# Kernel tuning notes

Measured on AMD Instinct MI355X. Metric: run time of the kernel, lower is better.

The kernel has to match this reference:

```python
import jax, jax.numpy as jnp
import numpy as np

B, N, H, HEADS = 4, 4096, 256, 8
DEG = 16
E = B * N * DEG  # 262144 edges
DH = H // HEADS


def setup_inputs() -> dict:
    key = jax.random.key(0)
    ks = jax.random.split(key, 8)
    node_states = jax.random.normal(ks[0], (B, N, H), dtype=jnp.float32)
    # edge_indices rows: [batch_idx, target_node, source_node]
    b_idx = jnp.repeat(jnp.arange(B, dtype=jnp.int64), N * DEG)
    tgt = jnp.tile(jnp.repeat(jnp.arange(N, dtype=jnp.int64), DEG), B)
    src = jax.random.randint(ks[1], (E,), 0, N, dtype=jnp.int64)
    edge_indices = jnp.stack([b_idx, tgt, src])  # (3, E)
    s = 1.0 / np.sqrt(H)
    Wq = jax.random.normal(ks[2], (H, H), dtype=jnp.float32) * s
    Wk = jax.random.normal(ks[3], (H, H), dtype=jnp.float32) * s
    Wv = jax.random.normal(ks[4], (H, H), dtype=jnp.float32) * s
    bq = jnp.zeros((H,), dtype=jnp.float32)
    bk = jnp.zeros((H,), dtype=jnp.float32)
    bv = jnp.zeros((H,), dtype=jnp.float32)
    return {"node_states": node_states, "edge_indices": edge_indices,
            "Wq": Wq, "bq": bq, "Wk": Wk, "bk": bk, "Wv": Wv, "bv": bv}


def reference(node_states, edge_indices, Wq, bq, Wk, bk, Wv, bv):
    batch, n_nodes, hidden = node_states.shape
    b_idx, tgt, src = edge_indices[0], edge_indices[1], edge_indices[2]
    num_edges = b_idx.shape[0]

    # Dense Q/K/V projections on nodes (cheap), then per-edge gathers.
    Q = (node_states @ Wq + bq).reshape(batch, n_nodes, HEADS, DH)
    K = (node_states @ Wk + bk).reshape(batch, n_nodes, HEADS, DH)
    V = (node_states @ Wv + bv).reshape(batch, n_nodes, HEADS, DH)

    q_e = Q[b_idx, tgt]  # (E, heads, dh)
    k_e = K[b_idx, src]  # (E, heads, dh)
    scores = jnp.sum(q_e * k_e, axis=-1) / jnp.sqrt(jnp.float32(DH))  # (E, heads)

    # Segment softmax over source nodes, grouped per (batch, target) --
    # mirrors torch.sparse.softmax(logits, dim=-2).
    seg = b_idx * n_nodes + tgt  # (E,)
    num_seg = batch * n_nodes
    m = jax.ops.segment_max(scores, seg, num_segments=num_seg)  # (B*N, heads)
    exp = jnp.exp(scores - m[seg])
    denom = jax.ops.segment_sum(exp, seg, num_segments=num_seg)
    attn = exp / denom[seg]  # (E, heads)

    # Weighted scatter-sum of source values into target nodes
    # (replaces sparse edge_mask @ elwise_prod).
    v_e = V[b_idx, src]  # (E, heads, dh)
    weighted = (attn[..., None] * v_e).reshape(num_edges, hidden)
    out = jax.ops.segment_sum(weighted, seg, num_segments=num_seg)
    return out.reshape(batch, n_nodes, hidden)
```

## Files before the change

kernel.cpp:

```cpp
#include <hip/hip_runtime.h>
#include <hip/hip_bf16.h>

#define BATCH 4
#define NNODES 4096
#define HID 256
#define NHEADS 8
#define DH 32
#define DEG 16
#define NEDGES (BATCH * NNODES * DEG)
#define NROWS (BATCH * NNODES)

typedef __attribute__((ext_vector_type(8))) short short8;
typedef __attribute__((ext_vector_type(8))) unsigned short ushort8;
typedef __attribute__((ext_vector_type(4))) unsigned short u16x4;
typedef __attribute__((ext_vector_type(4))) float f32x4;

static __device__ __forceinline__ unsigned short f2bf(float f) {
  __hip_bfloat16 h = __float2bfloat16(f);
  return *reinterpret_cast<unsigned short*>(&h);
}
static __device__ __forceinline__ float bf2f(unsigned short u) {
  unsigned int v = ((unsigned int)u) << 16;
  return *reinterpret_cast<float*>(&v);
}

__global__ __launch_bounds__(256) void w_prep_kernel(
    const float* __restrict__ Wq, const float* __restrict__ Wk,
    const float* __restrict__ Wv, unsigned short* __restrict__ Wt) {
  const int o = blockIdx.x * 2048 + threadIdx.x * 8;
  const int mat   = o >> 16;
  const int w     = o & 65535;
  const int strip = w >> 14;
  const int r     = w & 16383;
  const int kk    = r >> 11;
  const int hi    = (r >> 9) & 3;
  const int col   = (r >> 3) & 63;
  const int k0    = kk * 32 + hi * 8;
  const int c     = strip * 64 + col;
  const float* __restrict__ W = (mat == 0) ? Wq : (mat == 1) ? Wk : Wv;
  ushort8 ovec;
  #pragma unroll
  for (int j = 0; j < 8; ++j) {
    ovec[j] = f2bf(W[(size_t)(k0 + j) * HID + c]);
  }
  *reinterpret_cast<ushort8*>(&Wt[o]) = ovec;
}

__global__ __launch_bounds__(256, 4) void qkv_mfma_kernel(
    const float* __restrict__ X, const unsigned short* __restrict__ Wt,
    const float* __restrict__ bq, const float* __restrict__ bk,
    const float* __restrict__ bv,
    float* __restrict__ Qs, unsigned short* __restrict__ Kb,
    unsigned short* __restrict__ Vb) {
  __shared__ unsigned short sW[16384];

  const int tid = threadIdx.x;
  const int xcd = blockIdx.x & 7;
  const int l = blockIdx.x >> 3;
  const int cs = l & 3;
  const int chunk = (l >> 2) * 8 + xcd;
  const int c0 = cs * 64;

  const int lane = tid & 63;
  const int wv = tid >> 6;
  const int lm = lane & 15;
  const int hi = lane >> 4;
  const int lk = hi * 8;
  const int row = chunk * 64 + wv * 16 + lm;

  short8 Af[8];
  #pragma unroll
  for (int kk = 0; kk < 8; ++kk) {
    const float4 a0 = *reinterpret_cast<const float4*>(&X[(size_t)row * 256 + kk * 32 + lk]);
    const float4 a1 = *reinterpret_cast<const float4*>(&X[(size_t)row * 256 + kk * 32 + lk + 4]);
    short8 v;
    v[0] = (short)f2bf(a0.x); v[1] = (short)f2bf(a0.y);
    v[2] = (short)f2bf(a0.z); v[3] = (short)f2bf(a0.w);
    v[4] = (short)f2bf(a1.x); v[5] = (short)f2bf(a1.y);
    v[6] = (short)f2bf(a1.z); v[7] = (short)f2bf(a1.w);
    Af[kk] = v;
  }

  #pragma unroll
  for (int m = 0; m < 3; ++m) {
    const unsigned short* __restrict__ Wsrc = Wt + (size_t)(m * 4 + cs) * 16384;
    #pragma unroll
    for (int i = 0; i < 8; ++i) {
      const int e = i * 2048 + tid * 8;
      *reinterpret_cast<ushort8*>(&sW[e]) =
          *reinterpret_cast<const ushort8*>(&Wsrc[e]);
    }
    __syncthreads();

    const float* __restrict__ bias = (m == 0) ? bq : (m == 1) ? bk : bv;

    #pragma unroll
    for (int nt = 0; nt < 4; ++nt) {
      short8 Bf[8];
      #pragma unroll
      for (int kk = 0; kk < 8; ++kk) {
        Bf[kk] = *reinterpret_cast<const short8*>(
            &sW[kk * 2048 + hi * 512 + (nt * 16 + lm) * 8]);
      }
      f32x4 acc = {0.f, 0.f, 0.f, 0.f};
      #pragma unroll
      for (int kk = 0; kk < 8; ++kk) {
        acc = __builtin_amdgcn_mfma_f32_16x16x32_bf16(Bf[kk], Af[kk], acc, 0, 0, 0);
      }
      const int col0 = c0 + nt * 16 + hi * 4;
      const float4 b4 = *reinterpret_cast<const float4*>(&bias[col0]);
      if (m == 0) {
        float4 o;
        o.x = acc[0] + b4.x; o.y = acc[1] + b4.y;
        o.z = acc[2] + b4.z; o.w = acc[3] + b4.w;
        *reinterpret_cast<float4*>(&Qs[(size_t)row * 256 + col0]) = o;
      } else {
        u16x4 o;
        o[0] = f2bf(acc[0] + b4.x); o[1] = f2bf(acc[1] + b4.y);
        o[2] = f2bf(acc[2] + b4.z); o[3] = f2bf(acc[3] + b4.w);
        unsigned short* __restrict__ dst = (m == 1) ? Kb : Vb;
        *reinterpret_cast<u16x4*>(&dst[(size_t)row * 256 + col0]) = o;
      }
    }
    __syncthreads();
  }
}

__global__ __launch_bounds__(256) void attn_kernel(
    const float* __restrict__ Q, const unsigned short* __restrict__ K,
    const unsigned short* __restrict__ V, const int* __restrict__ edges,
    float* __restrict__ out) {
  __shared__ float s_w[DEG * NHEADS];

  const int bx = blockIdx.x;
  const int xcd = bx & 7;
  const int g = (xcd >> 1) * NNODES + (((bx >> 3) << 1) | (xcd & 1));
  const int e0 = g * DEG;
  const int tid = threadIdx.x;

  const int b = edges[e0];
  const int qrow = b * NNODES + edges[NEDGES + e0];

  const int lane = tid & 63;
  const int wv = tid >> 6;
  const int j = lane >> 2;
  const int hh = (lane >> 1) & 1;
  const int p = lane & 1;
  const int h = wv * 2 + hh;
  const int ch0 = h * 32 + p * 16;

  const int nsrc = b * NNODES + edges[2 * NEDGES + e0 + j];

  const float* __restrict__ qp = &Q[(size_t)qrow * HID + ch0];
  const float4 q0 = *reinterpret_cast<const float4*>(qp);
  const float4 q1 = *reinterpret_cast<const float4*>(qp + 4);
  const float4 q2 = *reinterpret_cast<const float4*>(qp + 8);
  const float4 q3 = *reinterpret_cast<const float4*>(qp + 12);
  const unsigned short* __restrict__ kp = &K[(size_t)nsrc * HID + ch0];
  const ushort8 k0 = *reinterpret_cast<const ushort8*>(kp);
  const ushort8 k1 = *reinterpret_cast<const ushort8*>(kp + 8);

  float partial;
  partial  = q0.x * bf2f(k0[0]); partial = fmaf(q0.y, bf2f(k0[1]), partial);
  partial = fmaf(q0.z, bf2f(k0[2]), partial); partial = fmaf(q0.w, bf2f(k0[3]), partial);
  partial = fmaf(q1.x, bf2f(k0[4]), partial); partial = fmaf(q1.y, bf2f(k0[5]), partial);
  partial = fmaf(q1.z, bf2f(k0[6]), partial); partial = fmaf(q1.w, bf2f(k0[7]), partial);
  partial = fmaf(q2.x, bf2f(k1[0]), partial); partial = fmaf(q2.y, bf2f(k1[1]), partial);
  partial = fmaf(q2.z, bf2f(k1[2]), partial); partial = fmaf(q2.w, bf2f(k1[3]), partial);
  partial = fmaf(q3.x, bf2f(k1[4]), partial); partial = fmaf(q3.y, bf2f(k1[5]), partial);
  partial = fmaf(q3.z, bf2f(k1[6]), partial); partial = fmaf(q3.w, bf2f(k1[7]), partial);

  partial += __shfl_xor(partial, 1);
  const float sc = partial * 0.17677669529663687f;

  float mx = sc;
  mx = fmaxf(mx, __shfl_xor(mx, 4));
  mx = fmaxf(mx, __shfl_xor(mx, 8));
  mx = fmaxf(mx, __shfl_xor(mx, 16));
  mx = fmaxf(mx, __shfl_xor(mx, 32));
  const float e = __expf(sc - mx);
  float sum = e;
  sum += __shfl_xor(sum, 4);
  sum += __shfl_xor(sum, 8);
  sum += __shfl_xor(sum, 16);
  sum += __shfl_xor(sum, 32);

  if (p == 0) s_w[j * NHEADS + h] = e / sum;
  __syncthreads();

  const int h3 = tid >> 5;
  float acc = 0.0f;
  #pragma unroll
  for (int jj = 0; jj < DEG; ++jj) {
    const int n = b * NNODES + edges[2 * NEDGES + e0 + jj];
    acc = fmaf(s_w[jj * NHEADS + h3], bf2f(V[(size_t)n * HID + tid]), acc);
  }
  out[(size_t)qrow * HID + tid] = acc;
}

extern "C" void kernel_launch(void* const* d_in, const int* in_sizes, int n_in,
                              void* d_out, int out_size, void* d_ws, size_t ws_size,
                              hipStream_t stream) {
  const float* X     = (const float*)d_in[0];
  const int*   edges = (const int*)d_in[1];
  const float* Wq    = (const float*)d_in[2];
  const float* bq    = (const float*)d_in[3];
  const float* Wk    = (const float*)d_in[4];
  const float* bk    = (const float*)d_in[5];
  const float* Wv    = (const float*)d_in[6];
  const float* bv    = (const float*)d_in[7];
  float* out = (float*)d_out;

  char* w = (char*)d_ws;
  float*          Qs = (float*)w;                 w += (size_t)NROWS * HID * 4;
  unsigned short* Kb = (unsigned short*)w;        w += (size_t)NROWS * HID * 2;
  unsigned short* Vb = (unsigned short*)w;        w += (size_t)NROWS * HID * 2;
  unsigned short* Wt = (unsigned short*)w;

  w_prep_kernel<<<96, 256, 0, stream>>>(Wq, Wk, Wv, Wt);
  qkv_mfma_kernel<<<1024, 256, 0, stream>>>(X, Wt, bq, bk, bv, Qs, Kb, Vb);
  attn_kernel<<<NROWS, 256, 0, stream>>>(Qs, Kb, Vb, edges, out);
}
```

Measured before the change: 63.38 us.

## Pre-convert X to bf16, read weights from global, drop attention barrier

The prep kernel now also converts the node states X to bf16 in a separate pass. The QKV MFMA kernel then loads bf16 fragments directly, so its four column-strip blocks read half-size activations instead of re-converting fp32. Weight tiles are read straight from global memory and cache instead of being staged through LDS, which removes the LDS copies and two block barriers per matrix. In the attention kernel, each wave reads only the softmax weights it wrote itself, so the block barrier is replaced by an LDS wait counter. The cost is an extra full read and write pass over X, and weight-fragment loads now go through global memory and cache rather than LDS.

```diff
diff --git a/kernel.cpp b/kernel.cpp
--- a/kernel.cpp
+++ b/kernel.cpp
@@ -24,36 +24,49 @@
   return *reinterpret_cast<float*>(&v);
 }
 
-__global__ __launch_bounds__(256) void w_prep_kernel(
+#define XBLOCKS 2048
+#define WBLOCKS 96
+__global__ __launch_bounds__(256) void prep_kernel(
+    const float* __restrict__ X,
     const float* __restrict__ Wq, const float* __restrict__ Wk,
-    const float* __restrict__ Wv, unsigned short* __restrict__ Wt) {
-  const int o = blockIdx.x * 2048 + threadIdx.x * 8;
-  const int mat   = o >> 16;
-  const int w     = o & 65535;
-  const int strip = w >> 14;
-  const int r     = w & 16383;
-  const int kk    = r >> 11;
-  const int hi    = (r >> 9) & 3;
-  const int col   = (r >> 3) & 63;
-  const int k0    = kk * 32 + hi * 8;
-  const int c     = strip * 64 + col;
-  const float* __restrict__ W = (mat == 0) ? Wq : (mat == 1) ? Wk : Wv;
-  ushort8 ovec;
-  #pragma unroll
-  for (int j = 0; j < 8; ++j) {
-    ovec[j] = f2bf(W[(size_t)(k0 + j) * HID + c]);
-  }
-  *reinterpret_cast<ushort8*>(&Wt[o]) = ovec;
+    const float* __restrict__ Wv,
+    unsigned short* __restrict__ Xb, unsigned short* __restrict__ Wt) {
+  const int tid = threadIdx.x;
+  if (blockIdx.x < XBLOCKS) {
+    const size_t base = (size_t)blockIdx.x * 2048 + (size_t)tid * 8;
+    const float4 a = *reinterpret_cast<const float4*>(&X[base]);
+    const float4 b = *reinterpret_cast<const float4*>(&X[base + 4]);
+    ushort8 o;
+    o[0] = f2bf(a.x); o[1] = f2bf(a.y); o[2] = f2bf(a.z); o[3] = f2bf(a.w);
+    o[4] = f2bf(b.x); o[5] = f2bf(b.y); o[6] = f2bf(b.z); o[7] = f2bf(b.w);
+    *reinterpret_cast<ushort8*>(&Xb[base]) = o;
+  } else {
+    const int o = (blockIdx.x - XBLOCKS) * 2048 + tid * 8;
+    const int mat   = o >> 16;
+    const int w     = o & 65535;
+    const int strip = w >> 14;
+    const int r     = w & 16383;
+    const int kk    = r >> 11;
+    const int hi    = (r >> 9) & 3;
+    const int col   = (r >> 3) & 63;
+    const int k0    = kk * 32 + hi * 8;
+    const int c     = strip * 64 + col;
+    const float* __restrict__ W = (mat == 0) ? Wq : (mat == 1) ? Wk : Wv;
+    ushort8 ovec;
+    #pragma unroll
+    for (int j = 0; j < 8; ++j) {
+      ovec[j] = f2bf(W[(size_t)(k0 + j) * HID + c]);
+    }
+    *reinterpret_cast<ushort8*>(&Wt[o]) = ovec;
+  }
 }
 
 __global__ __launch_bounds__(256, 4) void qkv_mfma_kernel(
-    const float* __restrict__ X, const unsigned short* __restrict__ Wt,
+    const unsigned short* __restrict__ Xb, const unsigned short* __restrict__ Wt,
     const float* __restrict__ bq, const float* __restrict__ bk,
     const float* __restrict__ bv,
     float* __restrict__ Qs, unsigned short* __restrict__ Kb,
     unsigned short* __restrict__ Vb) {
-  __shared__ unsigned short sW[16384];
-
   const int tid = threadIdx.x;
   const int xcd = blockIdx.x & 7;
   const int l = blockIdx.x >> 3;
@@ -71,27 +84,13 @@
   short8 Af[8];
   #pragma unroll
   for (int kk = 0; kk < 8; ++kk) {
-    const float4 a0 = *reinterpret_cast<const float4*>(&X[(size_t)row * 256 + kk * 32 + lk]);
-    const float4 a1 = *reinterpret_cast<const float4*>(&X[(size_t)row * 256 + kk * 32 + lk + 4]);
-    short8 v;
-    v[0] = (short)f2bf(a0.x); v[1] = (short)f2bf(a0.y);
-    v[2] = (short)f2bf(a0.z); v[3] = (short)f2bf(a0.w);
-    v[4] = (short)f2bf(a1.x); v[5] = (short)f2bf(a1.y);
-    v[6] = (short)f2bf(a1.z); v[7] = (short)f2bf(a1.w);
-    Af[kk] = v;
+    Af[kk] = *reinterpret_cast<const short8*>(
+        &Xb[(size_t)row * 256 + kk * 32 + lk]);
   }
 
   #pragma unroll
   for (int m = 0; m < 3; ++m) {
-    const unsigned short* __restrict__ Wsrc = Wt + (size_t)(m * 4 + cs) * 16384;
-    #pragma unroll
-    for (int i = 0; i < 8; ++i) {
-      const int e = i * 2048 + tid * 8;
-      *reinterpret_cast<ushort8*>(&sW[e]) =
-          *reinterpret_cast<const ushort8*>(&Wsrc[e]);
-    }
-    __syncthreads();
-
+    const unsigned short* __restrict__ Wm = Wt + (size_t)(m * 4 + cs) * 16384;
     const float* __restrict__ bias = (m == 0) ? bq : (m == 1) ? bk : bv;
 
     #pragma unroll
@@ -100,7 +99,7 @@
       #pragma unroll
       for (int kk = 0; kk < 8; ++kk) {
         Bf[kk] = *reinterpret_cast<const short8*>(
-            &sW[kk * 2048 + hi * 512 + (nt * 16 + lm) * 8]);
+            &Wm[kk * 2048 + hi * 512 + (nt * 16 + lm) * 8]);
       }
       f32x4 acc = {0.f, 0.f, 0.f, 0.f};
       #pragma unroll
@@ -122,7 +121,6 @@
         *reinterpret_cast<u16x4*>(&dst[(size_t)row * 256 + col0]) = o;
       }
     }
-    __syncthreads();
   }
 }
 
@@ -186,7 +184,7 @@
   sum += __shfl_xor(sum, 32);
 
   if (p == 0) s_w[j * NHEADS + h] = e / sum;
-  __syncthreads();
+  asm volatile("s_waitcnt lgkmcnt(0)" ::: "memory");
 
   const int h3 = tid >> 5;
   float acc = 0.0f;
@@ -215,9 +213,10 @@
   float*          Qs = (float*)w;                 w += (size_t)NROWS * HID * 4;
   unsigned short* Kb = (unsigned short*)w;        w += (size_t)NROWS * HID * 2;
   unsigned short* Vb = (unsigned short*)w;        w += (size_t)NROWS * HID * 2;
+  unsigned short* Xb = (unsigned short*)w;        w += (size_t)NROWS * HID * 2;
   unsigned short* Wt = (unsigned short*)w;
 
-  w_prep_kernel<<<96, 256, 0, stream>>>(Wq, Wk, Wv, Wt);
-  qkv_mfma_kernel<<<1024, 256, 0, stream>>>(X, Wt, bq, bk, bv, Qs, Kb, Vb);
+  prep_kernel<<<XBLOCKS + WBLOCKS, 256, 0, stream>>>(X, Wq, Wk, Wv, Xb, Wt);
+  qkv_mfma_kernel<<<1024, 256, 0, stream>>>(Xb, Wt, bq, bk, bv, Qs, Kb, Vb);
   attn_kernel<<<NROWS, 256, 0, stream>>>(Qs, Kb, Vb, edges, out);
 }
```

Measured after the change: 65.17 us. +2.8%, slower.
